# Kernel optimization log

Measured on AMD Instinct MI355X. Metric: run time of the kernel, lower is better.

Reference implementation:

```python
import jax, jax.numpy as jnp
import numpy as np

N, F, G, E, L, HID, C = 16384, 256, 64, 131072, 3, 512, 2
EPS = 1e-5
IU = F * (F - 1) // 2      # 32640 strict-upper-tri features per graph
IN1 = IU + F * L           # 33408 MLP input width


def setup_inputs() -> dict:
    key = jax.random.key(0)
    ks = jax.random.split(key, 16)

    def w(k, shape, fan_in):
        return jax.random.normal(k, shape, jnp.float32) * (1.0 / np.sqrt(fan_in))

    return {
        "x": jax.random.normal(ks[0], (N, F), jnp.float32),
        "edge_index": jax.random.randint(ks[1], (2, E), 0, N, dtype=jnp.int32),
        "batch": jnp.repeat(jnp.arange(G, dtype=jnp.int32), N // G),  # F nodes per graph
        "lin_src_w": w(ks[2], (L, F, F), F), "lin_src_b": jnp.zeros((L, F), jnp.float32),
        "lin_dst_w": w(ks[3], (L, F, F), F), "lin_dst_b": jnp.zeros((L, F), jnp.float32),
        "att_w": w(ks[4], (L, 2 * F, 1), 2 * F), "att_b": jnp.zeros((L, 1), jnp.float32),
        "bn_g": jnp.ones((IU,), jnp.float32), "bn_b": jnp.zeros((IU,), jnp.float32),
        "bnh_g": jnp.ones((F * L,), jnp.float32), "bnh_b": jnp.zeros((F * L,), jnp.float32),
        "w1": w(ks[5], (IN1, HID), IN1), "b1": jnp.zeros((HID,), jnp.float32),
        "g1": jnp.ones((HID,), jnp.float32), "be1": jnp.zeros((HID,), jnp.float32),
        "w2": w(ks[6], (HID, HID // 2), HID), "b2": jnp.zeros((HID // 2,), jnp.float32),
        "g2": jnp.ones((HID // 2,), jnp.float32), "be2": jnp.zeros((HID // 2,), jnp.float32),
        "w3": w(ks[7], (HID // 2, HID // 2), HID // 2), "b3": jnp.zeros((HID // 2,), jnp.float32),
        "g3": jnp.ones((HID // 2,), jnp.float32), "be3": jnp.zeros((HID // 2,), jnp.float32),
        "w4": w(ks[8], (HID // 2, C), HID // 2), "b4": jnp.zeros((C,), jnp.float32),
    }


def _bn(z, g, b):
    # BatchNorm1d (training-mode batch stats, biased variance, as torch uses for normalization)
    m = jnp.mean(z, 0)
    v = jnp.var(z, 0)
    return (z - m) * jax.lax.rsqrt(v + EPS) * g + b


def _conv(x, src, dst, Ws, bs, Wd, bd, Wa, ba):
    # EdgeLevelAttention layer (heads=1): gather -> concat -> linear -> softmax(heads) -> weighted scatter-add
    x_src = x @ Ws + bs                      # [N, F]
    x_dst = x @ Wd + bd                      # [N, F]
    x_j = x_src[src]                         # [E2, F] source features per edge
    x_i = x_dst[dst]                         # [E2, F] destination features per edge
    alpha = jax.nn.softmax(jnp.concatenate([x_i, x_j], -1) @ Wa + ba, axis=1)  # [E2, 1] (all ones for heads=1)
    msg = x_i * alpha                        # message uses x_i, as in the source
    return jax.ops.segment_sum(msg, dst, num_segments=N)


def reference(x, edge_index, batch, lin_src_w, lin_src_b, lin_dst_w, lin_dst_b,
              att_w, att_b, bn_g, bn_b, bnh_g, bnh_b,
              w1, b1, g1, be1, w2, b2, g2, be2, w3, b3, g3, be3, w4, b4):
    loops = jnp.arange(N, dtype=edge_index.dtype)          # add_self_loops
    src = jnp.concatenate([edge_index[0], loops])
    dst = jnp.concatenate([edge_index[1], loops])

    h = x
    pooled = []
    cnt = jax.ops.segment_sum(jnp.ones((N, 1), x.dtype), batch, num_segments=G)
    for l in range(L):
        h = _conv(h, src, dst, lin_src_w[l], lin_src_b[l],
                  lin_dst_w[l], lin_dst_b[l], att_w[l], att_b[l])
        pooled.append(jax.ops.segment_sum(h, batch, num_segments=G) / cnt)  # global_mean_pool

    iu = np.triu_indices(F, k=1)
    xt = x.reshape(G, F, F)[:, iu[0], iu[1]]               # strict upper triangle per graph [G, IU]
    xt = _bn(xt, bn_g, bn_b)
    hh = _bn(jnp.concatenate(pooled, 1), bnh_g, bnh_b)     # [G, F*L]
    z = jnp.concatenate([xt, hh], 1)                       # [G, IN1]

    z = jax.nn.relu(_bn(z @ w1 + b1, g1, be1))
    z = jax.nn.relu(_bn(z @ w2 + b2, g2, be2))
    z = jax.nn.relu(_bn(z @ w3 + b3, g3, be3))
    return z @ w4 + b4                                     # [G, C]
```

## Files before the change

### kernel.cpp

```cpp
#include <hip/hip_runtime.h>
#include <cstdint>

typedef __attribute__((ext_vector_type(8))) short short8;
typedef __attribute__((ext_vector_type(4))) float f32x4;
typedef unsigned short ushort_t;

static constexpr int NN = 16384, FF = 256, GG = 64, EE = 131072, LL = 3;
static constexpr int HIDN = 512, IU = 32640, IN1 = 33408;
#define EPSV 1e-5f

__device__ inline unsigned short bf16r(float v) {
  unsigned u = __float_as_uint(v);
  u += 0x7FFFu + ((u >> 16) & 1u);
  return (unsigned short)(u >> 16);
}

__global__ __launch_bounds__(256) void k_zero(int* __restrict__ p) {
  int i = blockIdx.x * 256 + threadIdx.x;
  if (i < 16448) p[i] = 0;
}

__global__ __launch_bounds__(256) void k_hist(const int* __restrict__ dst,
                                              const int* __restrict__ batch,
                                              int* __restrict__ deg, int* __restrict__ cnt) {
  __shared__ int hist[64];
  int bx = blockIdx.x, t = threadIdx.x;
  if (bx < 512) {
    int e = bx * 256 + t;
    atomicAdd(&deg[dst[e]], 1);
  } else {
    if (t < 64) hist[t] = 0;
    __syncthreads();
    int4 v = ((const int4*)batch)[(bx - 512) * 256 + t];
    int a[4] = {v.x, v.y, v.z, v.w};
    int cur = a[0], run = 1;
#pragma unroll
    for (int j = 1; j < 4; ++j) {
      if (a[j] == cur) run++;
      else { atomicAdd(&hist[cur], run); cur = a[j]; run = 1; }
    }
    atomicAdd(&hist[cur], run);
    __syncthreads();
    if (t < 64 && hist[t]) atomicAdd(&cnt[t], hist[t]);
  }
}

__global__ __launch_bounds__(256, 2) void k_conv(const float* __restrict__ A,
                                                 const float* __restrict__ W,
                                                 const float* __restrict__ bias,
                                                 const int* __restrict__ deg,
                                                 float* __restrict__ C,
                                                 float* __restrict__ pooled_p, int lofs) {
  __shared__ __align__(16) unsigned short Ah[64][72], Al[64][72];
  __shared__ __align__(16) unsigned short Bh[128][72], Bl[128][72];
  int mb = blockIdx.x;
  int n0 = blockIdx.y * 128, m0 = mb * 64;
  int t = threadIdx.x;
  int w = t >> 6, l = t & 63;
  int wn = w * 32;
  int lr = l & 15, lg = l >> 4;
  f32x4 acc[4][2];
#pragma unroll
  for (int fm = 0; fm < 4; ++fm)
#pragma unroll
    for (int fn = 0; fn < 2; ++fn) acc[fm][fn] = (f32x4){0.f, 0.f, 0.f, 0.f};

  int am = t >> 2, aq = t & 3;
  int bkp = t & 3, bnf = (t >> 2) & 31, brr = t >> 7;

  for (int ks = 0; ks < 4; ++ks) {
    int k0 = ks * 64;
    if (ks) __syncthreads();
    {
      const float* ap = A + (size_t)(m0 + am) * FF + k0;
#pragma unroll
      for (int i = 0; i < 4; ++i) {
        int k = aq * 4 + i * 16;
        float4 v = *(const float4*)(ap + k);
        const float* vf = (const float*)&v;
        unsigned short h[4], lo[4];
#pragma unroll
        for (int j = 0; j < 4; ++j) {
          h[j] = bf16r(vf[j]);
          lo[j] = bf16r(vf[j] - __uint_as_float((unsigned)h[j] << 16));
        }
        *(uint2*)&Ah[am][k] = make_uint2((unsigned)h[0] | ((unsigned)h[1] << 16),
                                         (unsigned)h[2] | ((unsigned)h[3] << 16));
        *(uint2*)&Al[am][k] = make_uint2((unsigned)lo[0] | ((unsigned)lo[1] << 16),
                                         (unsigned)lo[2] | ((unsigned)lo[3] << 16));
      }
    }
#pragma unroll
    for (int r2 = 0; r2 < 4; ++r2) {
      int k = 2 * bkp + 8 * (brr * 4 + r2);
      const float* wp = W + (size_t)(k0 + k) * FF + n0 + bnf * 4;
      float4 va = *(const float4*)wp;
      float4 vb = *(const float4*)(wp + FF);
      const float* fa = (const float*)&va;
      const float* fb = (const float*)&vb;
#pragma unroll
      for (int j = 0; j < 4; ++j) {
        unsigned short ha = bf16r(fa[j]), hb = bf16r(fb[j]);
        unsigned short la = bf16r(fa[j] - __uint_as_float((unsigned)ha << 16));
        unsigned short lb = bf16r(fb[j] - __uint_as_float((unsigned)hb << 16));
        int n = bnf * 4 + j;
        *(unsigned*)&Bh[n][k] = (unsigned)ha | ((unsigned)hb << 16);
        *(unsigned*)&Bl[n][k] = (unsigned)la | ((unsigned)lb << 16);
      }
    }
    __syncthreads();
#pragma unroll
    for (int k2 = 0; k2 < 2; ++k2) {
      int kk = k2 * 32 + lg * 8;
      short8 afh[4], afl[4], bfh[2], bfl[2];
#pragma unroll
      for (int fm = 0; fm < 4; ++fm) {
        afh[fm] = *(const short8*)&Ah[fm * 16 + lr][kk];
        afl[fm] = *(const short8*)&Al[fm * 16 + lr][kk];
      }
#pragma unroll
      for (int fn = 0; fn < 2; ++fn) {
        bfh[fn] = *(const short8*)&Bh[wn + fn * 16 + lr][kk];
        bfl[fn] = *(const short8*)&Bl[wn + fn * 16 + lr][kk];
      }
#pragma unroll
      for (int fm = 0; fm < 4; ++fm)
#pragma unroll
        for (int fn = 0; fn < 2; ++fn) {
          acc[fm][fn] = __builtin_amdgcn_mfma_f32_16x16x32_bf16(afl[fm], bfh[fn], acc[fm][fn], 0, 0, 0);
          acc[fm][fn] = __builtin_amdgcn_mfma_f32_16x16x32_bf16(afh[fm], bfl[fn], acc[fm][fn], 0, 0, 0);
          acc[fm][fn] = __builtin_amdgcn_mfma_f32_16x16x32_bf16(afh[fm], bfh[fn], acc[fm][fn], 0, 0, 0);
        }
    }
  }
  float degf[4][4];
#pragma unroll
  for (int fm = 0; fm < 4; ++fm)
#pragma unroll
    for (int r = 0; r < 4; ++r)
      degf[fm][r] = (float)(deg[m0 + fm * 16 + lg * 4 + r] + 1);
  int g = mb >> 2, sub = mb & 3;
#pragma unroll
  for (int fn = 0; fn < 2; ++fn) {
    int col = n0 + wn + fn * 16 + lr;
    float bb = bias[col];
    float cs = 0.f;
#pragma unroll
    for (int fm = 0; fm < 4; ++fm) {
      const float* av = (const float*)&acc[fm][fn];
#pragma unroll
      for (int r = 0; r < 4; ++r) {
        int row = m0 + fm * 16 + lg * 4 + r;
        float v = (av[r] + bb) * degf[fm][r];
        if (C) C[(size_t)row * FF + col] = v;
        cs += v;
      }
    }
    cs += __shfl_xor(cs, 16);
    cs += __shfl_xor(cs, 32);
    if (lg == 0)
      pooled_p[((size_t)sub * 64 + g) * (FF * LL) + lofs + col] = cs;
  }
}

__global__ __launch_bounds__(1024, 1) void k_bn_front(const float* __restrict__ x,
                                                      const float* __restrict__ bn_g,
                                                      const float* __restrict__ bn_b,
                                                      const float* __restrict__ pooled_p,
                                                      const int* __restrict__ cnt,
                                                      const float* __restrict__ bnh_g,
                                                      const float* __restrict__ bnh_b,
                                                      ushort_t* __restrict__ zh,
                                                      ushort_t* __restrict__ zl) {
  if (blockIdx.x < 256) {
    __shared__ float sb1[16][256], sb2[16][256];
    __shared__ float rsA[256], bbA[256];
    int i = blockIdx.x, t = threadIdx.x;
    int jq = t & 63, gq = t >> 6;
    int j4 = jq * 4;
    float4 vals[4];
    float s1[4] = {}, s2[4] = {};
#pragma unroll
    for (int r = 0; r < 4; ++r) {
      int g = gq * 4 + r;
      float4 vv = *(const float4*)(x + (size_t)(g * 256 + i) * FF + j4);
      vals[r] = vv;
      s1[0] += vv.x; s2[0] += vv.x * vv.x;
      s1[1] += vv.y; s2[1] += vv.y * vv.y;
      s1[2] += vv.z; s2[2] += vv.z * vv.z;
      s1[3] += vv.w; s2[3] += vv.w * vv.w;
    }
    *(float4*)&sb1[gq][j4] = make_float4(s1[0], s1[1], s1[2], s1[3]);
    *(float4*)&sb2[gq][j4] = make_float4(s2[0], s2[1], s2[2], s2[3]);
    __syncthreads();
    if (t < 256) {
      int j = t;
      float S1 = 0.f, S2 = 0.f;
#pragma unroll
      for (int q = 0; q < 16; ++q) { S1 += sb1[q][j]; S2 += sb2[q][j]; }
      float m = S1 * (1.f / 64.f);
      float var = S2 * (1.f / 64.f) - m * m;
      float rs = 0.f, bb = 0.f;
      if (j > i) {
        int p = i * 255 - (i * (i - 1)) / 2 + (j - i - 1);
        rs = rsqrtf(var + EPSV) * bn_g[p];
        bb = bn_b[p] - m * rs;
      }
      rsA[j] = rs;
      bbA[j] = bb;
    }
    __syncthreads();
    int P0 = i * 255 - (i * (i - 1)) / 2 - i - 1;
#pragma unroll
    for (int r = 0; r < 4; ++r) {
      int g = gq * 4 + r;
      size_t base = (size_t)g * IN1 + P0;
      const float* vf = (const float*)&vals[r];
#pragma unroll
      for (int jj = 0; jj < 4; ++jj) {
        int j = j4 + jj;
        if (j > i) {
          float f = vf[jj] * rsA[j] + bbA[j];
          unsigned short h = bf16r(f);
          zh[base + j] = h;
          zl[base + j] = bf16r(f - __uint_as_float((unsigned)h << 16));
        }
      }
    }
  } else {
    __shared__ float pb1[4][64], pb2[4][64], prs[64], pbb[64];
    int t = threadIdx.x;
    if (t >= 256) return;
    int bx = blockIdx.x - 256;
    int ql = t & 63, gq = t >> 6;
    int q = bx * 64 + ql;
    float vals[16];
    float s1 = 0.f, s2 = 0.f;
#pragma unroll
    for (int gg = 0; gg < 16; ++gg) {
      int g = gq * 16 + gg;
      float v = (pooled_p[((size_t)0 * 64 + g) * (FF * LL) + q] +
                 pooled_p[((size_t)1 * 64 + g) * (FF * LL) + q] +
                 pooled_p[((size_t)2 * 64 + g) * (FF * LL) + q] +
                 pooled_p[((size_t)3 * 64 + g) * (FF * LL) + q]) / (float)cnt[g];
      vals[gg] = v;
      s1 += v;
      s2 += v * v;
    }
    pb1[gq][ql] = s1;
    pb2[gq][ql] = s2;
    __syncthreads();
    if (t < 64) {
      float S1 = pb1[0][t] + pb1[1][t] + pb1[2][t] + pb1[3][t];
      float S2 = pb2[0][t] + pb2[1][t] + pb2[2][t] + pb2[3][t];
      float m = S1 * (1.f / 64.f);
      float var = S2 * (1.f / 64.f) - m * m;
      int qq = bx * 64 + t;
      float rs = rsqrtf(var + EPSV) * bnh_g[qq];
      prs[t] = rs;
      pbb[t] = bnh_b[qq] - m * rs;
    }
    __syncthreads();
#pragma unroll
    for (int gg = 0; gg < 16; ++gg) {
      int g = gq * 16 + gg;
      float f = vals[gg] * prs[ql] + pbb[ql];
      unsigned short h = bf16r(f);
      zh[(size_t)g * IN1 + IU + q] = h;
      zl[(size_t)g * IN1 + IU + q] = bf16r(f - __uint_as_float((unsigned)h << 16));
    }
  }
}

__global__ __launch_bounds__(256, 4) void k_w1(const ushort_t* __restrict__ zh,
                                               const ushort_t* __restrict__ zl,
                                               const float* __restrict__ W,
                                               float* __restrict__ partial) {
  __shared__ __align__(16) unsigned short Zh[64][72], Zl[64][72];
  __shared__ __align__(16) unsigned short Wh[64][72], Wl[64][72];
  int nb = blockIdx.x, s = blockIdx.y;
  int t = threadIdx.x;
  int w = t >> 6, l = t & 63, lr = l & 15, lg = l >> 4;
  int ncol = nb * 64 + w * 16 + lr;
  f32x4 acc[4];
#pragma unroll
  for (int mt = 0; mt < 4; ++mt) acc[mt] = (f32x4){0.f, 0.f, 0.f, 0.f};

  for (int c = s; c < 522; c += 128) {
    int p0 = c * 64;
    if (c != s) __syncthreads();
#pragma unroll
    for (int it = 0; it < 2; ++it) {
      int idx = it * 256 + t;
      int g = idx >> 3, kq = idx & 7;
      *(uint4*)&Zh[g][kq * 8] = *(const uint4*)(zh + (size_t)g * IN1 + p0 + kq * 8);
      *(uint4*)&Zl[g][kq * 8] = *(const uint4*)(zl + (size_t)g * IN1 + p0 + kq * 8);
    }
#pragma unroll
    for (int it = 0; it < 2; ++it) {
      int idx = it * 256 + t;
      int kp = idx >> 4, cg = idx & 15;
      int k = kp * 2;
      const float* wp = W + (size_t)(p0 + k) * HIDN + nb * 64 + cg * 4;
      float4 va = *(const float4*)wp;
      float4 vb = *(const float4*)(wp + HIDN);
      const float* fa = (const float*)&va;
      const float* fb = (const float*)&vb;
#pragma unroll
      for (int j = 0; j < 4; ++j) {
        unsigned ua = __float_as_uint(fa[j]);
        unsigned ub = __float_as_uint(fb[j]);
        unsigned short ha = (unsigned short)(ua >> 16);
        unsigned short hb = (unsigned short)(ub >> 16);
        unsigned short la = bf16r(fa[j] - __uint_as_float(ua & 0xFFFF0000u));
        unsigned short lb = bf16r(fb[j] - __uint_as_float(ub & 0xFFFF0000u));
        int col = cg * 4 + j;
        *(unsigned*)&Wh[col][k] = (unsigned)ha | ((unsigned)hb << 16);
        *(unsigned*)&Wl[col][k] = (unsigned)la | ((unsigned)lb << 16);
      }
    }
    __syncthreads();
#pragma unroll
    for (int k2 = 0; k2 < 2; ++k2) {
      int kloc = k2 * 32 + lg * 8;
      short8 bh = *(const short8*)&Wh[w * 16 + lr][kloc];
      short8 bl = *(const short8*)&Wl[w * 16 + lr][kloc];
#pragma unroll
      for (int mt = 0; mt < 4; ++mt) {
        short8 ah = *(const short8*)&Zh[mt * 16 + lr][kloc];
        short8 al = *(const short8*)&Zl[mt * 16 + lr][kloc];
        acc[mt] = __builtin_amdgcn_mfma_f32_16x16x32_bf16(al, bh, acc[mt], 0, 0, 0);
        acc[mt] = __builtin_amdgcn_mfma_f32_16x16x32_bf16(ah, bl, acc[mt], 0, 0, 0);
        acc[mt] = __builtin_amdgcn_mfma_f32_16x16x32_bf16(ah, bh, acc[mt], 0, 0, 0);
      }
    }
  }
#pragma unroll
  for (int mt = 0; mt < 4; ++mt) {
    const float* av = (const float*)&acc[mt];
#pragma unroll
    for (int r = 0; r < 4; ++r) {
      int g = mt * 16 + lg * 4 + r;
      partial[((size_t)s * 64 + g) * HIDN + ncol] = av[r];
    }
  }
}

__global__ __launch_bounds__(256) void k_reduce(const float* __restrict__ partial,
                                                const float* __restrict__ bias,
                                                float* __restrict__ out, int S, int N) {
  int idx = blockIdx.x * 256 + threadIdx.x;
  if (idx >= 64 * N) return;
  int h = idx % N;
  float a = bias[h];
  for (int s = 0; s < S; ++s) a += partial[(size_t)s * 64 * N + idx];
  out[idx] = a;
}

__global__ __launch_bounds__(64) void k_bn_relu(const float* __restrict__ in,
                                                const float* __restrict__ gamma,
                                                const float* __restrict__ beta,
                                                float* __restrict__ out, int N) {
  int h = blockIdx.x;
  int g = threadIdx.x;
  float v = in[(size_t)g * N + h];
  float s = v, s2 = v * v;
#pragma unroll
  for (int o = 32; o > 0; o >>= 1) {
    s += __shfl_xor(s, o);
    s2 += __shfl_xor(s2, o);
  }
  float m = s * (1.f / 64.f);
  float var = s2 * (1.f / 64.f) - m * m;
  float r = (v - m) * rsqrtf(var + EPSV) * gamma[h] + beta[h];
  out[(size_t)g * N + h] = fmaxf(r, 0.f);
}

__global__ __launch_bounds__(256, 2) void k_mlp_small(const float* __restrict__ Z,
                                                      const float* __restrict__ W,
                                                      const float* __restrict__ bias,
                                                      const float* __restrict__ gamma,
                                                      const float* __restrict__ beta,
                                                      float* __restrict__ out, int K, int N) {
  __shared__ float Ws[512 * 16];
  __shared__ float zl[64][132];
  __shared__ float sb1[16][17], sb2[16][17];
  int t = threadIdx.x;
  int h0 = blockIdx.x * 16;
  for (int idx = t; idx < K * 4; idx += 256) {
    int r = idx >> 2, q = idx & 3;
    *(float4*)&Ws[r * 16 + q * 4] = *(const float4*)(W + (size_t)r * N + h0 + q * 4);
  }
  int c = t & 15, gq = t >> 4;
  float acc[4] = {};
  for (int ch = 0; ch < K; ch += 128) {
    for (int idx = t; idx < 64 * 32; idx += 256) {
      int g = idx >> 5, kq = idx & 31;
      *(float4*)&zl[g][kq * 4] = *(const float4*)(Z + (size_t)g * K + ch + kq * 4);
    }
    __syncthreads();
#pragma unroll 8
    for (int kk = 0; kk < 128; ++kk) {
      float w = Ws[(ch + kk) * 16 + c];
#pragma unroll
      for (int i = 0; i < 4; ++i) acc[i] = fmaf(zl[gq * 4 + i][kk], w, acc[i]);
    }
    __syncthreads();
  }
  float bb = bias[h0 + c];
  float s1 = 0.f, s2 = 0.f;
#pragma unroll
  for (int i = 0; i < 4; ++i) {
    acc[i] += bb;
    s1 += acc[i];
    s2 += acc[i] * acc[i];
  }
  sb1[gq][c] = s1;
  sb2[gq][c] = s2;
  __syncthreads();
  float S1 = 0.f, S2 = 0.f;
#pragma unroll
  for (int q = 0; q < 16; ++q) { S1 += sb1[q][c]; S2 += sb2[q][c]; }
  float m = S1 * (1.f / 64.f);
  float var = S2 * (1.f / 64.f) - m * m;
  float rs = rsqrtf(var + EPSV) * gamma[h0 + c];
  float be = beta[h0 + c];
#pragma unroll
  for (int i = 0; i < 4; ++i)
    out[(size_t)(gq * 4 + i) * N + h0 + c] = fmaxf((acc[i] - m) * rs + be, 0.f);
}

__global__ __launch_bounds__(256) void k_final(const float* __restrict__ A,
                                               const float* __restrict__ w4,
                                               const float* __restrict__ b4,
                                               float* __restrict__ out) {
  __shared__ float w4l[512];
  int t = threadIdx.x;
  w4l[t] = w4[t];
  w4l[256 + t] = w4[256 + t];
  __syncthreads();
  int w = t >> 6, l = t & 63;
  for (int g = w * 16; g < w * 16 + 16; ++g) {
    float4 av = *(const float4*)(A + (size_t)g * 256 + l * 4);
    float c0 = av.x * w4l[(l * 4 + 0) * 2] + av.y * w4l[(l * 4 + 1) * 2] +
               av.z * w4l[(l * 4 + 2) * 2] + av.w * w4l[(l * 4 + 3) * 2];
    float c1 = av.x * w4l[(l * 4 + 0) * 2 + 1] + av.y * w4l[(l * 4 + 1) * 2 + 1] +
               av.z * w4l[(l * 4 + 2) * 2 + 1] + av.w * w4l[(l * 4 + 3) * 2 + 1];
#pragma unroll
    for (int o = 32; o > 0; o >>= 1) {
      c0 += __shfl_xor(c0, o);
      c1 += __shfl_xor(c1, o);
    }
    if (l == 0) {
      out[g * 2 + 0] = c0 + b4[0];
      out[g * 2 + 1] = c1 + b4[1];
    }
  }
}

extern "C" void kernel_launch(void* const* d_in, const int* in_sizes, int n_in,
                              void* d_out, int out_size, void* d_ws, size_t ws_size,
                              hipStream_t stream) {
  const float* x = (const float*)d_in[0];
  const int* edge = (const int*)d_in[1];
  const int* batch = (const int*)d_in[2];
  const float* lin_dst_w = (const float*)d_in[5];
  const float* lin_dst_b = (const float*)d_in[6];
  const float* bn_g = (const float*)d_in[9];
  const float* bn_b = (const float*)d_in[10];
  const float* bnh_g = (const float*)d_in[11];
  const float* bnh_b = (const float*)d_in[12];
  const float* w1 = (const float*)d_in[13];
  const float* b1 = (const float*)d_in[14];
  const float* g1 = (const float*)d_in[15];
  const float* be1 = (const float*)d_in[16];
  const float* w2 = (const float*)d_in[17];
  const float* b2 = (const float*)d_in[18];
  const float* g2 = (const float*)d_in[19];
  const float* be2 = (const float*)d_in[20];
  const float* w3 = (const float*)d_in[21];
  const float* b3 = (const float*)d_in[22];
  const float* g3 = (const float*)d_in[23];
  const float* be3 = (const float*)d_in[24];
  const float* w4 = (const float*)d_in[25];
  const float* b4 = (const float*)d_in[26];
  const int* dstp = edge + EE;

  char* ws = (char*)d_ws;
  int* deg = (int*)(ws);
  int* cnt = (int*)(ws + 65536);
  float* bufA = (float*)(ws + 131072);
  float* bufB = (float*)(ws + 131072 + 16777216);
  float* pooled_p = (float*)(ws + 131072 + 2 * 16777216);
  char* tail = ws + 131072 + 2 * 16777216 + 786432;
  float* m1 = (float*)(tail);
  float* m1b = (float*)(tail + 131072);
  float* m2b = (float*)(tail + 262144);
  float* m3b = (float*)(tail + 262144 + 65536);
  ushort_t* zh = (ushort_t*)bufA;
  ushort_t* zlp = zh + (size_t)64 * IN1;
  float* partial = bufB;

  k_zero<<<65, 256, 0, stream>>>(deg);
  k_hist<<<528, 256, 0, stream>>>(dstp, batch, deg, cnt);

  k_conv<<<dim3(256, 2), 256, 0, stream>>>(x, lin_dst_w, lin_dst_b, deg, bufA, pooled_p, 0);
  k_conv<<<dim3(256, 2), 256, 0, stream>>>(bufA, lin_dst_w + (size_t)FF * FF,
                                           lin_dst_b + FF, deg, bufB, pooled_p, FF);
  k_conv<<<dim3(256, 2), 256, 0, stream>>>(bufB, lin_dst_w + (size_t)2 * FF * FF,
                                           lin_dst_b + 2 * FF, deg, (float*)nullptr,
                                           pooled_p, 2 * FF);

  k_bn_front<<<268, 1024, 0, stream>>>(x, bn_g, bn_b, pooled_p, cnt, bnh_g, bnh_b, zh, zlp);

  k_w1<<<dim3(8, 128), 256, 0, stream>>>(zh, zlp, w1, partial);
  k_reduce<<<128, 256, 0, stream>>>(partial, b1, m1, 128, HIDN);
  k_bn_relu<<<HIDN, 64, 0, stream>>>(m1, g1, be1, m1b, HIDN);

  k_mlp_small<<<16, 256, 0, stream>>>(m1b, w2, b2, g2, be2, m2b, HIDN, 256);
  k_mlp_small<<<16, 256, 0, stream>>>(m2b, w3, b3, g3, be3, m3b, 256, 256);

  k_final<<<1, 256, 0, stream>>>(m3b, w4, b4, (float*)d_out);
}
```

Baseline: 187.3 us.

## Store conv outputs as pre-split bf16 pairs, fuse BN-ReLU into MLP, halve W1 split

The conv epilogue now writes each intermediate as a packed 32-bit word holding the truncated high bf16 and the rounded residual low bf16, so the next layer reads the hi/lo split directly instead of recomputing it. The conv grid is transposed so the two column blocks of the same row tile launch adjacently. The separate BN+ReLU kernel after the first MLP layer is folded into the second MLP kernel's input staging, which removes one launch and one round trip. The W1 split-K is reduced from 128 to 64 slices, giving fewer partials to reduce but less parallelism per block.

```diff
diff --git a/kernel.cpp b/kernel.cpp
--- a/kernel.cpp
+++ b/kernel.cpp
@@ -45,16 +45,16 @@
   }
 }
 
-__global__ __launch_bounds__(256, 2) void k_conv(const float* __restrict__ A,
+template <int SIN>
+__global__ __launch_bounds__(256, 2) void k_conv(const void* __restrict__ Ap,
                                                  const float* __restrict__ W,
                                                  const float* __restrict__ bias,
                                                  const int* __restrict__ deg,
-                                                 float* __restrict__ C,
+                                                 unsigned* __restrict__ Cpk,
                                                  float* __restrict__ pooled_p, int lofs) {
   __shared__ __align__(16) unsigned short Ah[64][72], Al[64][72];
   __shared__ __align__(16) unsigned short Bh[128][72], Bl[128][72];
-  int mb = blockIdx.x;
-  int n0 = blockIdx.y * 128, m0 = mb * 64;
+  int n0 = blockIdx.x * 128, m0 = blockIdx.y * 64;
   int t = threadIdx.x;
   int w = t >> 6, l = t & 63;
   int wn = w * 32;
@@ -71,8 +71,8 @@
   for (int ks = 0; ks < 4; ++ks) {
     int k0 = ks * 64;
     if (ks) __syncthreads();
-    {
-      const float* ap = A + (size_t)(m0 + am) * FF + k0;
+    if (SIN == 0) {
+      const float* ap = (const float*)Ap + (size_t)(m0 + am) * FF + k0;
 #pragma unroll
       for (int i = 0; i < 4; ++i) {
         int k = aq * 4 + i * 16;
@@ -89,6 +89,24 @@
         *(uint2*)&Al[am][k] = make_uint2((unsigned)lo[0] | ((unsigned)lo[1] << 16),
                                          (unsigned)lo[2] | ((unsigned)lo[3] << 16));
       }
+    } else {
+      const unsigned* ap = (const unsigned*)Ap + (size_t)(m0 + am) * FF + k0;
+#pragma unroll
+      for (int i = 0; i < 4; ++i) {
+        int k = aq * 4 + i * 16;
+        uint4 v = *(const uint4*)(ap + k);
+        const unsigned* vu = (const unsigned*)&v;
+        unsigned short h[4], lo[4];
+#pragma unroll
+        for (int j = 0; j < 4; ++j) {
+          h[j] = (unsigned short)(vu[j] >> 16);
+          lo[j] = (unsigned short)vu[j];
+        }
+        *(uint2*)&Ah[am][k] = make_uint2((unsigned)h[0] | ((unsigned)h[1] << 16),
+                                         (unsigned)h[2] | ((unsigned)h[3] << 16));
+        *(uint2*)&Al[am][k] = make_uint2((unsigned)lo[0] | ((unsigned)lo[1] << 16),
+                                         (unsigned)lo[2] | ((unsigned)lo[3] << 16));
+      }
     }
 #pragma unroll
     for (int r2 = 0; r2 < 4; ++r2) {
@@ -139,7 +157,7 @@
 #pragma unroll
     for (int r = 0; r < 4; ++r)
       degf[fm][r] = (float)(deg[m0 + fm * 16 + lg * 4 + r] + 1);
-  int g = mb >> 2, sub = mb & 3;
+  int g = blockIdx.y >> 2, sub = blockIdx.y & 3;
 #pragma unroll
   for (int fn = 0; fn < 2; ++fn) {
     int col = n0 + wn + fn * 16 + lr;
@@ -152,8 +170,13 @@
       for (int r = 0; r < 4; ++r) {
         int row = m0 + fm * 16 + lg * 4 + r;
         float v = (av[r] + bb) * degf[fm][r];
-        if (C) C[(size_t)row * FF + col] = v;
         cs += v;
+        if (Cpk) {
+          unsigned uv = __float_as_uint(v);
+          unsigned hi = uv & 0xFFFF0000u;
+          unsigned short lo16 = bf16r(v - __uint_as_float(hi));
+          Cpk[(size_t)row * FF + col] = hi | (unsigned)lo16;
+        }
       }
     }
     cs += __shfl_xor(cs, 16);
@@ -286,7 +309,7 @@
 #pragma unroll
   for (int mt = 0; mt < 4; ++mt) acc[mt] = (f32x4){0.f, 0.f, 0.f, 0.f};
 
-  for (int c = s; c < 522; c += 128) {
+  for (int c = s; c < 522; c += 64) {
     int p0 = c * 64;
     if (c != s) __syncthreads();
 #pragma unroll
@@ -357,26 +380,10 @@
   out[idx] = a;
 }
 
-__global__ __launch_bounds__(64) void k_bn_relu(const float* __restrict__ in,
-                                                const float* __restrict__ gamma,
-                                                const float* __restrict__ beta,
-                                                float* __restrict__ out, int N) {
-  int h = blockIdx.x;
-  int g = threadIdx.x;
-  float v = in[(size_t)g * N + h];
-  float s = v, s2 = v * v;
-#pragma unroll
-  for (int o = 32; o > 0; o >>= 1) {
-    s += __shfl_xor(s, o);
-    s2 += __shfl_xor(s2, o);
-  }
-  float m = s * (1.f / 64.f);
-  float var = s2 * (1.f / 64.f) - m * m;
-  float r = (v - m) * rsqrtf(var + EPSV) * gamma[h] + beta[h];
-  out[(size_t)g * N + h] = fmaxf(r, 0.f);
-}
-
+template <int INBN>
 __global__ __launch_bounds__(256, 2) void k_mlp_small(const float* __restrict__ Z,
+                                                      const float* __restrict__ ibn_g,
+                                                      const float* __restrict__ ibn_b,
                                                       const float* __restrict__ W,
                                                       const float* __restrict__ bias,
                                                       const float* __restrict__ gamma,
@@ -399,6 +406,25 @@
       *(float4*)&zl[g][kq * 4] = *(const float4*)(Z + (size_t)g * K + ch + kq * 4);
     }
     __syncthreads();
+    if (INBN) {
+      if (t < 128) {
+        float s1 = 0.f, s2 = 0.f;
+#pragma unroll
+        for (int g = 0; g < 64; ++g) {
+          float v = zl[g][t];
+          s1 += v;
+          s2 += v * v;
+        }
+        float m = s1 * (1.f / 64.f);
+        float var = s2 * (1.f / 64.f) - m * m;
+        float rs = rsqrtf(var + EPSV) * ibn_g[ch + t];
+        float bb = ibn_b[ch + t] - m * rs;
+#pragma unroll
+        for (int g = 0; g < 64; ++g)
+          zl[g][t] = fmaxf(zl[g][t] * rs + bb, 0.f);
+      }
+      __syncthreads();
+    }
 #pragma unroll 8
     for (int kk = 0; kk < 128; ++kk) {
       float w = Ws[(ch + kk) * 16 + c];
@@ -494,9 +520,8 @@
   float* pooled_p = (float*)(ws + 131072 + 2 * 16777216);
   char* tail = ws + 131072 + 2 * 16777216 + 786432;
   float* m1 = (float*)(tail);
-  float* m1b = (float*)(tail + 131072);
-  float* m2b = (float*)(tail + 262144);
-  float* m3b = (float*)(tail + 262144 + 65536);
+  float* m2b = (float*)(tail + 131072);
+  float* m3b = (float*)(tail + 131072 + 65536);
   ushort_t* zh = (ushort_t*)bufA;
   ushort_t* zlp = zh + (size_t)64 * IN1;
   float* partial = bufB;
@@ -504,21 +529,22 @@
   k_zero<<<65, 256, 0, stream>>>(deg);
   k_hist<<<528, 256, 0, stream>>>(dstp, batch, deg, cnt);
 
-  k_conv<<<dim3(256, 2), 256, 0, stream>>>(x, lin_dst_w, lin_dst_b, deg, bufA, pooled_p, 0);
-  k_conv<<<dim3(256, 2), 256, 0, stream>>>(bufA, lin_dst_w + (size_t)FF * FF,
-                                           lin_dst_b + FF, deg, bufB, pooled_p, FF);
-  k_conv<<<dim3(256, 2), 256, 0, stream>>>(bufB, lin_dst_w + (size_t)2 * FF * FF,
-                                           lin_dst_b + 2 * FF, deg, (float*)nullptr,
-                                           pooled_p, 2 * FF);
+  k_conv<0><<<dim3(2, 256), 256, 0, stream>>>(x, lin_dst_w, lin_dst_b, deg,
+                                              (unsigned*)bufA, pooled_p, 0);
+  k_conv<1><<<dim3(2, 256), 256, 0, stream>>>(bufA, lin_dst_w + (size_t)FF * FF,
+                                              lin_dst_b + FF, deg, (unsigned*)bufB,
+                                              pooled_p, FF);
+  k_conv<1><<<dim3(2, 256), 256, 0, stream>>>(bufB, lin_dst_w + (size_t)2 * FF * FF,
+                                              lin_dst_b + 2 * FF, deg, (unsigned*)nullptr,
+                                              pooled_p, 2 * FF);
 
   k_bn_front<<<268, 1024, 0, stream>>>(x, bn_g, bn_b, pooled_p, cnt, bnh_g, bnh_b, zh, zlp);
 
-  k_w1<<<dim3(8, 128), 256, 0, stream>>>(zh, zlp, w1, partial);
-  k_reduce<<<128, 256, 0, stream>>>(partial, b1, m1, 128, HIDN);
-  k_bn_relu<<<HIDN, 64, 0, stream>>>(m1, g1, be1, m1b, HIDN);
-
-  k_mlp_small<<<16, 256, 0, stream>>>(m1b, w2, b2, g2, be2, m2b, HIDN, 256);
-  k_mlp_small<<<16, 256, 0, stream>>>(m2b, w3, b3, g3, be3, m3b, 256, 256);
+  k_w1<<<dim3(8, 64), 256, 0, stream>>>(zh, zlp, w1, partial);
+  k_reduce<<<128, 256, 0, stream>>>(partial, b1, m1, 64, HIDN);
+
+  k_mlp_small<1><<<16, 256, 0, stream>>>(m1, g1, be1, w2, b2, g2, be2, m2b, HIDN, 256);
+  k_mlp_small<0><<<16, 256, 0, stream>>>(m2b, nullptr, nullptr, w3, b3, g3, be3, m3b, 256, 256);
 
   k_final<<<1, 256, 0, stream>>>(m3b, w4, b4, (float*)d_out);
 }
```

Measured after the change: 173.2 us. -7.5%, faster.
